# Optimization experiments

Hardware: AMD Instinct MI355X
Metric: run time of the kernel (lower is better)

## Reference

```python
import jax, jax.numpy as jnp
import numpy as np

N = 100000
E = 1600000
F_DIM = 128
H_DIM = 64
K_CLUSTERS = 16
NEG_SLOPE = 0.2


def setup_inputs() -> dict:
    key = jax.random.key(0)
    ks = jax.random.split(key, 10)
    X = jax.random.normal(ks[0], (N, F_DIM), dtype=jnp.float32)
    ei_feat = jax.random.randint(ks[1], (2, E), 0, N, dtype=jnp.int64)
    batch = jnp.zeros((N,), dtype=jnp.int64)
    # GATv2Conv layer 1 params (heads=1): lin_l, lin_r [F,H], att [H], bias [H]
    s1 = 1.0 / np.sqrt(F_DIM)
    W1l = jax.random.uniform(ks[2], (F_DIM, H_DIM), jnp.float32, -s1, s1)
    W1r = jax.random.uniform(ks[3], (F_DIM, H_DIM), jnp.float32, -s1, s1)
    a1 = jax.random.uniform(ks[4], (H_DIM,), jnp.float32, -1/np.sqrt(H_DIM), 1/np.sqrt(H_DIM))
    b1 = jnp.zeros((H_DIM,), jnp.float32)
    # layer 2: [H,K]
    s2 = 1.0 / np.sqrt(H_DIM)
    W2l = jax.random.uniform(ks[5], (H_DIM, K_CLUSTERS), jnp.float32, -s2, s2)
    W2r = jax.random.uniform(ks[6], (H_DIM, K_CLUSTERS), jnp.float32, -s2, s2)
    a2 = jax.random.uniform(ks[7], (K_CLUSTERS,), jnp.float32, -1/np.sqrt(K_CLUSTERS), 1/np.sqrt(K_CLUSTERS))
    b2 = jnp.zeros((K_CLUSTERS,), jnp.float32)
    return {"X": X, "ei_feat": ei_feat, "batch": batch,
            "W1l": W1l, "W1r": W1r, "a1": a1, "b1": b1,
            "W2l": W2l, "W2r": W2r, "a2": a2, "b2": b2}


def gatv2_conv(x, src, dst, Wl, Wr, a, b, n_nodes):
    # GATv2 (heads=1): e_ij = a^T LeakyReLU(Wl x_j + Wr x_i); softmax over j->i; out_i = sum alpha * Wl x_j
    xl = x @ Wl            # [N,H] source transform
    xr = x @ Wr            # [N,H] target transform
    e = jax.nn.leaky_relu(xl[src] + xr[dst], NEG_SLOPE) @ a   # [E']
    m = jax.ops.segment_max(e, dst, num_segments=n_nodes)      # stable softmax per target
    w = jnp.exp(e - m[dst])
    denom = jax.ops.segment_sum(w, dst, num_segments=n_nodes)
    alpha = w / denom[dst]  # every node has a self-loop, so denom > 0
    out = jax.ops.segment_sum(alpha[:, None] * xl[src], dst, num_segments=n_nodes)
    return out + b


def reference(X, ei_feat, batch, W1l, W1r, a1, b1, W2l, W2r, a2, b2):
    loop = jnp.arange(N, dtype=ei_feat.dtype)
    src = jnp.concatenate([ei_feat[0], loop])  # add_self_loops=True (PyG default)
    dst = jnp.concatenate([ei_feat[1], loop])
    h = jax.nn.elu(gatv2_conv(X, src, dst, W1l, W1r, a1, b1, N))
    z = gatv2_conv(h, src, dst, W2l, W2r, a2, b2, N)
    return jax.nn.softmax(z, axis=1)
```

## Files before the change

### kernel.cpp

```cpp
#include <hip/hip_runtime.h>
#include <stdint.h>

#define F_DIM 128
#define H_DIM 64
#define K_DIM 16
#define BUK_SH 8
#define NCH 256

typedef _Float16 half2v __attribute__((ext_vector_type(2)));
typedef _Float16 half4 __attribute__((ext_vector_type(4)));
typedef _Float16 f16x8 __attribute__((ext_vector_type(8)));
typedef float f32x4 __attribute__((ext_vector_type(4)));

__global__ __launch_bounds__(256) void k_hist(const int* __restrict__ dst,
                                              int* __restrict__ hist,
                                              int E, int CH, int NBUK) {
    __shared__ int h[512];
    int t = threadIdx.x, c = blockIdx.x;
    for (int i = t; i < NBUK; i += 256) h[i] = 0;
    __syncthreads();
    int s = c * CH, e = min(s + CH, E);
    for (int i = s + t; i < e; i += 256) atomicAdd(&h[dst[i] >> BUK_SH], 1);
    __syncthreads();
    for (int i = t; i < NBUK; i += 256) hist[i * NCH + c] = h[i];
}

__global__ __launch_bounds__(256) void k_scanBkt(int* __restrict__ hist,
                                                 int* __restrict__ bktTot) {
    __shared__ int sh[256];
    int b = blockIdx.x, t = threadIdx.x;
    int v = hist[b * NCH + t];
    sh[t] = v;
    __syncthreads();
    for (int off = 1; off < 256; off <<= 1) {
        int x = (t >= off) ? sh[t - off] : 0;
        __syncthreads();
        sh[t] += x;
        __syncthreads();
    }
    hist[b * NCH + t] = sh[t] - v;
    if (t == 255) bktTot[b] = sh[255];
}

__global__ __launch_bounds__(256) void k_scanTot(const int* __restrict__ bktTot,
                                                 int* __restrict__ bktBase, int NBUK) {
    __shared__ int sh[256];
    int t = threadIdx.x;
    int i0 = 2 * t, i1 = 2 * t + 1;
    int v0 = (i0 < NBUK) ? bktTot[i0] : 0;
    int v1 = (i1 < NBUK) ? bktTot[i1] : 0;
    int s = v0 + v1;
    sh[t] = s;
    __syncthreads();
    for (int off = 1; off < 256; off <<= 1) {
        int x = (t >= off) ? sh[t - off] : 0;
        __syncthreads();
        sh[t] += x;
        __syncthreads();
    }
    int excl = sh[t] - s;
    if (i0 < NBUK) bktBase[i0] = excl;
    if (i1 < NBUK) bktBase[i1] = excl + v0;
    if (t == 255) bktBase[NBUK] = sh[255];
}

__global__ __launch_bounds__(256) void k_scatter(const int* __restrict__ src,
                                                 const int* __restrict__ dst,
                                                 const int* __restrict__ hist,
                                                 const int* __restrict__ bktBase,
                                                 uint32_t* __restrict__ binned,
                                                 int E, int CH, int NBUK) {
    __shared__ int ctr[512];
    int t = threadIdx.x, c = blockIdx.x;
    for (int i = t; i < NBUK; i += 256) ctr[i] = bktBase[i] + hist[i * NCH + c];
    __syncthreads();
    int s = c * CH, e = min(s + CH, E);
    for (int i = s + t; i < e; i += 256) {
        int d = dst[i];
        int pos = atomicAdd(&ctr[d >> BUK_SH], 1);
        binned[pos] = (uint32_t)src[i] | ((uint32_t)(d & 255) << 20);
    }
}

__global__ __launch_bounds__(256) void k_fine2(const uint32_t* __restrict__ binned,
                                               const int* __restrict__ bktBase,
                                               int* __restrict__ rowptr,
                                               int* __restrict__ col, int N) {
    __shared__ int h[256], sc[256], slotL[256];
    int b = blockIdx.x, t = threadIdx.x;
    int n0 = b << BUK_SH;
    int s = bktBase[b], e = bktBase[b + 1];
    h[t] = 0;
    __syncthreads();
    for (int i = s + t; i < e; i += 256) atomicAdd(&h[binned[i] >> 20], 1);
    __syncthreads();
    int v = h[t];
    sc[t] = v;
    __syncthreads();
    for (int off = 1; off < 256; off <<= 1) {
        int x = (t >= off) ? sc[t - off] : 0;
        __syncthreads();
        sc[t] += x;
        __syncthreads();
    }
    int excl = sc[t] - v;
    int n = n0 + t;
    int rowbase = s + n0;
    if (n < N) {
        int rp = rowbase + excl + t;
        rowptr[n] = rp;
        col[rp] = n;
        slotL[t] = rp + 1;
        if (n == N - 1) rowptr[N] = rp + v + 1;
    }
    __syncthreads();
    for (int i = s + t; i < e; i += 256) {
        uint32_t p = binned[i];
        int pos = atomicAdd(&slotL[p >> 20], 1);
        col[pos] = (int)(p & 0xFFFFFu);
    }
}

__global__ __launch_bounds__(256) void k_gemm1m(
        const float* __restrict__ X,
        const float* __restrict__ W1l, const float* __restrict__ W1r,
        _Float16* __restrict__ xlh, _Float16* __restrict__ xrh, int N) {
    __shared__ _Float16 Ws[16384];
    __shared__ _Float16 Xs[128 * 136];
    int t = threadIdx.x;
    int n0 = blockIdx.x * 128;
    int validRows = N - n0; if (validRows > 128) validRows = 128;
    for (int i = t; i < 4096; i += 256) {
        int k = i >> 5, c4 = (i & 31) << 2;
        float4 v = (c4 < 64) ? *(const float4*)&W1l[k * 64 + c4]
                             : *(const float4*)&W1r[k * 64 + (c4 - 64)];
        int s = k >> 5, q = (k >> 3) & 3, j = k & 7;
        float vv[4] = {v.x, v.y, v.z, v.w};
#pragma unroll
        for (int u = 0; u < 4; ++u) {
            int C = c4 + u, c = C >> 4, n = C & 15;
            Ws[(((c * 4 + s) * 4 + q) * 16 + n) * 8 + j] = (_Float16)vv[u];
        }
    }
    for (int i = t; i < 4096; i += 256) {
        int r = i >> 5, c4 = (i & 31) << 2;
        float4 v = {0.f, 0.f, 0.f, 0.f};
        if (r < validRows) v = *(const float4*)&X[(long)(n0 + r) * 128 + c4];
        half4 hv;
        hv.x = (_Float16)v.x; hv.y = (_Float16)v.y;
        hv.z = (_Float16)v.z; hv.w = (_Float16)v.w;
        *(half4*)&Xs[r * 136 + c4] = hv;
    }
    __syncthreads();
    int w = t >> 6, lane = t & 63;
    int m = lane & 15, q = lane >> 4;
    f32x4 acc[2][8];
#pragma unroll
    for (int a = 0; a < 2; ++a)
#pragma unroll
        for (int c = 0; c < 8; ++c) acc[a][c] = (f32x4){0.f, 0.f, 0.f, 0.f};
#pragma unroll
    for (int s = 0; s < 4; ++s) {
        f16x8 a0 = *(const f16x8*)&Xs[(w * 32 + m) * 136 + s * 32 + q * 8];
        f16x8 a1 = *(const f16x8*)&Xs[(w * 32 + 16 + m) * 136 + s * 32 + q * 8];
#pragma unroll
        for (int c = 0; c < 8; ++c) {
            f16x8 b = *(const f16x8*)&Ws[(((c * 4 + s) * 4 + q) * 16 + m) * 8];
            acc[0][c] = __builtin_amdgcn_mfma_f32_16x16x32_f16(a0, b, acc[0][c], 0, 0, 0);
            acc[1][c] = __builtin_amdgcn_mfma_f32_16x16x32_f16(a1, b, acc[1][c], 0, 0, 0);
        }
    }
#pragma unroll
    for (int sub = 0; sub < 2; ++sub)
#pragma unroll
    for (int c = 0; c < 8; ++c)
#pragma unroll
    for (int r = 0; r < 4; ++r) {
        int gn = n0 + w * 32 + sub * 16 + q * 4 + r;
        if (gn < N) {
            int C = c * 16 + m;
            _Float16 v = (_Float16)acc[sub][c][r];
            if (C < 64) xlh[(long)gn * 64 + C] = v;
            else        xrh[(long)gn * 64 + (C - 64)] = v;
        }
    }
}

__global__ __launch_bounds__(256) void k_gemm2m(
        const _Float16* __restrict__ Hm,
        const float* __restrict__ W2l, const float* __restrict__ W2r,
        _Float16* __restrict__ xlh, _Float16* __restrict__ xrh, int N) {
    __shared__ _Float16 Ws2[2048];
    __shared__ _Float16 Hs[256 * 72];
    int t = threadIdx.x;
    int n0 = blockIdx.x * 256;
    int validRows = N - n0; if (validRows > 256) validRows = 256;
    for (int i = t; i < 512; i += 256) {
        int k = i >> 3, c4 = (i & 7) << 2;
        float4 v = (c4 < 16) ? *(const float4*)&W2l[k * 16 + c4]
                             : *(const float4*)&W2r[k * 16 + (c4 - 16)];
        int s = k >> 5, q = (k >> 3) & 3, j = k & 7;
        float vv[4] = {v.x, v.y, v.z, v.w};
#pragma unroll
        for (int u = 0; u < 4; ++u) {
            int C = c4 + u, c = C >> 4, n = C & 15;
            Ws2[(((c * 2 + s) * 4 + q) * 16 + n) * 8 + j] = (_Float16)vv[u];
        }
    }
    for (int i = t; i < 2048; i += 256) {
        int r = i >> 3, c8 = (i & 7) << 3;
        f16x8 v = {0, 0, 0, 0, 0, 0, 0, 0};
        if (r < validRows) v = *(const f16x8*)&Hm[(long)(n0 + r) * 64 + c8];
        *(f16x8*)&Hs[r * 72 + c8] = v;
    }
    __syncthreads();
    int w = t >> 6, lane = t & 63;
    int m = lane & 15, q = lane >> 4;
    f32x4 acc[4][2];
#pragma unroll
    for (int a = 0; a < 4; ++a)
#pragma unroll
        for (int c = 0; c < 2; ++c) acc[a][c] = (f32x4){0.f, 0.f, 0.f, 0.f};
#pragma unroll
    for (int s = 0; s < 2; ++s) {
        f16x8 a[4];
#pragma unroll
        for (int sub = 0; sub < 4; ++sub)
            a[sub] = *(const f16x8*)&Hs[(w * 64 + sub * 16 + m) * 72 + s * 32 + q * 8];
#pragma unroll
        for (int c = 0; c < 2; ++c) {
            f16x8 b = *(const f16x8*)&Ws2[(((c * 2 + s) * 4 + q) * 16 + m) * 8];
#pragma unroll
            for (int sub = 0; sub < 4; ++sub)
                acc[sub][c] = __builtin_amdgcn_mfma_f32_16x16x32_f16(a[sub], b, acc[sub][c], 0, 0, 0);
        }
    }
#pragma unroll
    for (int sub = 0; sub < 4; ++sub)
#pragma unroll
    for (int c = 0; c < 2; ++c)
#pragma unroll
    for (int r = 0; r < 4; ++r) {
        int gn = n0 + w * 64 + sub * 16 + q * 4 + r;
        if (gn < N) {
            int C = c * 16 + m;
            _Float16 v = (_Float16)acc[sub][c][r];
            if (C < 16) xlh[(long)gn * 16 + C] = v;
            else        xrh[(long)gn * 16 + (C - 16)] = v;
        }
    }
}

__global__ void k_att1(const f16x8* __restrict__ xlh, const f16x8* __restrict__ xrh,
                       const float* __restrict__ a1, const float* __restrict__ b1,
                       const int* __restrict__ rowptr, const int* __restrict__ col,
                       f16x8* __restrict__ hout, int N) {
    int n = (int)((blockIdx.x * (unsigned)blockDim.x + threadIdx.x) >> 4);
    int lane = threadIdx.x & 63;
    if (n >= N) return;
    int q = lane & 7;
    int g = (lane >> 3) & 1;
    float4 af0 = ((const float4*)a1)[q * 2 + 0];
    float4 af1 = ((const float4*)a1)[q * 2 + 1];
    half2v a01 = {(_Float16)af0.x, (_Float16)af0.y};
    half2v a23 = {(_Float16)af0.z, (_Float16)af0.w};
    half2v a45 = {(_Float16)af1.x, (_Float16)af1.y};
    half2v a67 = {(_Float16)af1.z, (_Float16)af1.w};
    f16x8 xrv = xrh[(long)n * 8 + q];
    int jb = rowptr[n], je = rowptr[n + 1];
    float l = 0.f;
    float o[8] = {0.f, 0.f, 0.f, 0.f, 0.f, 0.f, 0.f, 0.f};
    int j = jb + g;
    for (; j + 2 < je; j += 4) {
        int s0 = col[j], s1 = col[j + 2];
        f16x8 xh0 = xlh[(long)s0 * 8 + q];
        f16x8 xh1 = xlh[(long)s1 * 8 + q];
        f16x8 t0 = xh0 + xrv, t1 = xh1 + xrv;
        f16x8 u0 = __builtin_elementwise_max(t0, t0 * (_Float16)0.2f);
        f16x8 u1 = __builtin_elementwise_max(t1, t1 * (_Float16)0.2f);
        half2v u0a = {u0[0], u0[1]}, u0b = {u0[2], u0[3]}, u0c = {u0[4], u0[5]}, u0d = {u0[6], u0[7]};
        half2v u1a = {u1[0], u1[1]}, u1b = {u1[2], u1[3]}, u1c = {u1[4], u1[5]}, u1d = {u1[6], u1[7]};
        float e0 = __builtin_amdgcn_fdot2(u0a, a01,
                    __builtin_amdgcn_fdot2(u0b, a23,
                     __builtin_amdgcn_fdot2(u0c, a45,
                      __builtin_amdgcn_fdot2(u0d, a67, 0.f, false), false), false), false);
        float e1 = __builtin_amdgcn_fdot2(u1a, a01,
                    __builtin_amdgcn_fdot2(u1b, a23,
                     __builtin_amdgcn_fdot2(u1c, a45,
                      __builtin_amdgcn_fdot2(u1d, a67, 0.f, false), false), false), false);
#pragma unroll
        for (int off = 1; off < 8; off <<= 1) {
            e0 += __shfl_xor(e0, off, 8);
            e1 += __shfl_xor(e1, off, 8);
        }
        float c0 = __expf(e0), c1 = __expf(e1);
        l += c0 + c1;
#pragma unroll
        for (int i = 0; i < 8; ++i)
            o[i] = fmaf(c0, (float)xh0[i], fmaf(c1, (float)xh1[i], o[i]));
    }
    for (; j < je; j += 2) {
        int s = col[j];
        f16x8 xh = xlh[(long)s * 8 + q];
        f16x8 t = xh + xrv;
        f16x8 u = __builtin_elementwise_max(t, t * (_Float16)0.2f);
        half2v ua = {u[0], u[1]}, ub = {u[2], u[3]}, uc = {u[4], u[5]}, ud = {u[6], u[7]};
        float e = __builtin_amdgcn_fdot2(ua, a01,
                   __builtin_amdgcn_fdot2(ub, a23,
                    __builtin_amdgcn_fdot2(uc, a45,
                     __builtin_amdgcn_fdot2(ud, a67, 0.f, false), false), false), false);
#pragma unroll
        for (int off = 1; off < 8; off <<= 1) e += __shfl_xor(e, off, 8);
        float c = __expf(e);
        l += c;
#pragma unroll
        for (int i = 0; i < 8; ++i) o[i] = fmaf(c, (float)xh[i], o[i]);
    }
    l += __shfl_xor(l, 8);
#pragma unroll
    for (int i = 0; i < 8; ++i) o[i] += __shfl_xor(o[i], 8);
    if (g == 0) {
        float4 bv0 = ((const float4*)b1)[q * 2 + 0];
        float4 bv1 = ((const float4*)b1)[q * 2 + 1];
        float bb[8] = {bv0.x, bv0.y, bv0.z, bv0.w, bv1.x, bv1.y, bv1.z, bv1.w};
        float rl = 1.f / l;
        f16x8 hv;
#pragma unroll
        for (int i = 0; i < 8; ++i) {
            float h = o[i] * rl + bb[i];
            h = (h > 0.f) ? h : (__expf(h) - 1.f);
            hv[i] = (_Float16)h;
        }
        hout[(long)n * 8 + q] = hv;
    }
}

__global__ void k_att2(const half4* __restrict__ xlh, const half4* __restrict__ xrh,
                       const float* __restrict__ a2, const float* __restrict__ b2v,
                       const int* __restrict__ rowptr, const int* __restrict__ col,
                       float* __restrict__ out, int N) {
    int n = (int)((blockIdx.x * (unsigned)blockDim.x + threadIdx.x) >> 4);
    int lane = threadIdx.x & 63;
    if (n >= N) return;
    int q = lane & 3;
    int g = (lane >> 2) & 3;
    float4 af = ((const float4*)a2)[q];
    half2v alo = {(_Float16)af.x, (_Float16)af.y};
    half2v ahi = {(_Float16)af.z, (_Float16)af.w};
    half4 xrv = xrh[(long)n * 4 + q];
    int jb = rowptr[n], je = rowptr[n + 1];
    float l = 0.f;
    float4 o = {0.f, 0.f, 0.f, 0.f};
    int j = jb + g;
    for (; j + 4 < je; j += 8) {
        int s0 = col[j], s1 = col[j + 4];
        half4 xh0 = xlh[(long)s0 * 4 + q];
        half4 xh1 = xlh[(long)s1 * 4 + q];
        half4 t0 = xh0 + xrv, t1 = xh1 + xrv;
        half4 u0 = __builtin_elementwise_max(t0, t0 * (_Float16)0.2f);
        half4 u1 = __builtin_elementwise_max(t1, t1 * (_Float16)0.2f);
        half2v u0lo = {u0.x, u0.y}, u0hi = {u0.z, u0.w};
        half2v u1lo = {u1.x, u1.y}, u1hi = {u1.z, u1.w};
        float e0 = __builtin_amdgcn_fdot2(u0lo, alo,
                    __builtin_amdgcn_fdot2(u0hi, ahi, 0.f, false), false);
        float e1 = __builtin_amdgcn_fdot2(u1lo, alo,
                    __builtin_amdgcn_fdot2(u1hi, ahi, 0.f, false), false);
        e0 += __shfl_xor(e0, 1, 4); e0 += __shfl_xor(e0, 2, 4);
        e1 += __shfl_xor(e1, 1, 4); e1 += __shfl_xor(e1, 2, 4);
        float c0 = __expf(e0), c1 = __expf(e1);
        l += c0 + c1;
        o.x = fmaf(c0, (float)xh0.x, fmaf(c1, (float)xh1.x, o.x));
        o.y = fmaf(c0, (float)xh0.y, fmaf(c1, (float)xh1.y, o.y));
        o.z = fmaf(c0, (float)xh0.z, fmaf(c1, (float)xh1.z, o.z));
        o.w = fmaf(c0, (float)xh0.w, fmaf(c1, (float)xh1.w, o.w));
    }
    for (; j < je; j += 4) {
        int s = col[j];
        half4 xh = xlh[(long)s * 4 + q];
        half4 t = xh + xrv;
        half4 u = __builtin_elementwise_max(t, t * (_Float16)0.2f);
        half2v ulo = {u.x, u.y}, uhi = {u.z, u.w};
        float e = __builtin_amdgcn_fdot2(ulo, alo,
                   __builtin_amdgcn_fdot2(uhi, ahi, 0.f, false), false);
        e += __shfl_xor(e, 1, 4);
        e += __shfl_xor(e, 2, 4);
        float c = __expf(e);
        l += c;
        o.x = fmaf(c, (float)xh.x, o.x);
        o.y = fmaf(c, (float)xh.y, o.y);
        o.z = fmaf(c, (float)xh.z, o.z);
        o.w = fmaf(c, (float)xh.w, o.w);
    }
#pragma unroll
    for (int off = 4; off <= 8; off <<= 1) {
        l   += __shfl_xor(l, off);
        o.x += __shfl_xor(o.x, off);
        o.y += __shfl_xor(o.y, off);
        o.z += __shfl_xor(o.z, off);
        o.w += __shfl_xor(o.w, off);
    }
    if (g == 0) {
        float4 bv = ((const float4*)b2v)[q];
        float rl = 1.f / l;
        float4 z;
        z.x = o.x * rl + bv.x;
        z.y = o.y * rl + bv.y;
        z.z = o.z * rl + bv.z;
        z.w = o.w * rl + bv.w;
        float mx = fmaxf(fmaxf(z.x, z.y), fmaxf(z.z, z.w));
        mx = fmaxf(mx, __shfl_xor(mx, 1, 4));
        mx = fmaxf(mx, __shfl_xor(mx, 2, 4));
        float4 ez;
        ez.x = __expf(z.x - mx); ez.y = __expf(z.y - mx);
        ez.z = __expf(z.z - mx); ez.w = __expf(z.w - mx);
        float ss = ez.x + ez.y + ez.z + ez.w;
        ss += __shfl_xor(ss, 1, 4);
        ss += __shfl_xor(ss, 2, 4);
        float rs = 1.f / ss;
        ez.x *= rs; ez.y *= rs; ez.z *= rs; ez.w *= rs;
        ((float4*)out)[(long)n * 4 + q] = ez;
    }
}

extern "C" void kernel_launch(void* const* d_in, const int* in_sizes, int n_in,
                              void* d_out, int out_size, void* d_ws, size_t ws_size,
                              hipStream_t stream) {
    const float* X   = (const float*)d_in[0];
    const int*   ei  = (const int*)d_in[1];
    const float* W1l = (const float*)d_in[3];
    const float* W1r = (const float*)d_in[4];
    const float* a1  = (const float*)d_in[5];
    const float* b1  = (const float*)d_in[6];
    const float* W2l = (const float*)d_in[7];
    const float* W2r = (const float*)d_in[8];
    const float* a2  = (const float*)d_in[9];
    const float* b2  = (const float*)d_in[10];

    int N = in_sizes[0] / F_DIM;
    int E = in_sizes[1] / 2;
    int M = E + N;
    int NBUK = (N + 255) >> BUK_SH;
    int NH = NBUK * NCH;
    int CH = (E + NCH - 1) / NCH;
    const int* srcv = ei;
    const int* dstv = ei + E;

    char* w = (char*)d_ws;
    size_t off = 0;
    auto alloc = [&](size_t bytes) -> char* {
        char* p = w + off;
        off = (off + bytes + 255) & ~(size_t)255;
        return p;
    };
    int* rowptr  = (int*)alloc((size_t)(N + 1) * sizeof(int));
    int* hist    = (int*)alloc((size_t)NH * sizeof(int));
    int* bktTot  = (int*)alloc((size_t)NBUK * sizeof(int));
    int* bktBase = (int*)alloc((size_t)(NBUK + 1) * sizeof(int));
    int* col     = (int*)alloc((size_t)M * sizeof(int));
    uint32_t* binned = (uint32_t*)alloc((size_t)E * sizeof(uint32_t));
    _Float16* xl1h = (_Float16*)alloc((size_t)N * H_DIM * 2);
    _Float16* xr1h = (_Float16*)alloc((size_t)N * H_DIM * 2);
    _Float16* h1h  = (_Float16*)alloc((size_t)N * H_DIM * 2);
    _Float16* xl2h = (_Float16*)alloc((size_t)N * K_DIM * 2);
    _Float16* xr2h = (_Float16*)alloc((size_t)N * K_DIM * 2);

    k_hist<<<NCH, 256, 0, stream>>>(dstv, hist, E, CH, NBUK);
    k_scanBkt<<<NBUK, 256, 0, stream>>>(hist, bktTot);
    k_scanTot<<<1, 256, 0, stream>>>(bktTot, bktBase, NBUK);
    k_scatter<<<NCH, 256, 0, stream>>>(srcv, dstv, hist, bktBase, binned, E, CH, NBUK);
    k_fine2<<<NBUK, 256, 0, stream>>>(binned, bktBase, rowptr, col, N);

    int g1Blocks = (N + 127) / 128;
    k_gemm1m<<<g1Blocks, 256, 0, stream>>>(X, W1l, W1r, xl1h, xr1h, N);
    int nodeBlocks16 = (N + 15) / 16;
    k_att1<<<nodeBlocks16, 256, 0, stream>>>((const f16x8*)xl1h, (const f16x8*)xr1h,
                                             a1, b1, rowptr, col, (f16x8*)h1h, N);
    int g2Blocks = (N + 255) / 256;
    k_gemm2m<<<g2Blocks, 256, 0, stream>>>(h1h, W2l, W2r, xl2h, xr2h, N);
    k_att2<<<nodeBlocks16, 256, 0, stream>>>((const half4*)xl2h, (const half4*)xr2h,
                                             a2, b2, rowptr, col, (float*)d_out, N);
}
```

Baseline: 247.1 us.

## Pre-swizzle weights once, load GEMM operands directly, and vectorize output stores

A new small kernel converts and swizzles both layers' weights to fp16 once into global memory, so each GEMM block no longer rebuilds the weight tile in LDS. The GEMM kernels now load activation fragments straight from global memory into registers instead of staging them through shared memory. This also removes the __syncthreads barrier. Outputs go through a per-wave LDS transpose so rows are written with 16-byte vector stores instead of scattered 2-byte stores. The trade-offs are one extra launch, weight reads coming from global/L2 per wave, and less coalesced direct X loads.

```diff
diff --git a/kernel.cpp b/kernel.cpp
--- a/kernel.cpp
+++ b/kernel.cpp
@@ -121,132 +121,149 @@
     }
 }
 
+__global__ __launch_bounds__(256) void k_swzW(const float* __restrict__ W1l,
+                                              const float* __restrict__ W1r,
+                                              const float* __restrict__ W2l,
+                                              const float* __restrict__ W2r,
+                                              _Float16* __restrict__ Wg1,
+                                              _Float16* __restrict__ Wg2) {
+    int t = threadIdx.x;
+    if (blockIdx.x == 0) {
+        for (int i = t; i < 4096; i += 256) {
+            int k = i >> 5, c4 = (i & 31) << 2;
+            float4 v = (c4 < 64) ? *(const float4*)&W1l[k * 64 + c4]
+                                 : *(const float4*)&W1r[k * 64 + (c4 - 64)];
+            int s = k >> 5, q = (k >> 3) & 3, j = k & 7;
+            float vv[4] = {v.x, v.y, v.z, v.w};
+#pragma unroll
+            for (int u = 0; u < 4; ++u) {
+                int C = c4 + u, c = C >> 4, n = C & 15;
+                Wg1[(((c * 4 + s) * 4 + q) * 16 + n) * 8 + j] = (_Float16)vv[u];
+            }
+        }
+    } else {
+        for (int i = t; i < 512; i += 256) {
+            int k = i >> 3, c4 = (i & 7) << 2;
+            float4 v = (c4 < 16) ? *(const float4*)&W2l[k * 16 + c4]
+                                 : *(const float4*)&W2r[k * 16 + (c4 - 16)];
+            int s = k >> 5, q = (k >> 3) & 3, j = k & 7;
+            float vv[4] = {v.x, v.y, v.z, v.w};
+#pragma unroll
+            for (int u = 0; u < 4; ++u) {
+                int C = c4 + u, c = C >> 4, n = C & 15;
+                Wg2[(((c * 2 + s) * 4 + q) * 16 + n) * 8 + j] = (_Float16)vv[u];
+            }
+        }
+    }
+}
+
 __global__ __launch_bounds__(256) void k_gemm1m(
-        const float* __restrict__ X,
-        const float* __restrict__ W1l, const float* __restrict__ W1r,
+        const float* __restrict__ X, const _Float16* __restrict__ Wg,
         _Float16* __restrict__ xlh, _Float16* __restrict__ xrh, int N) {
-    __shared__ _Float16 Ws[16384];
-    __shared__ _Float16 Xs[128 * 136];
+    __shared__ _Float16 T[4][32 * 136];
     int t = threadIdx.x;
     int n0 = blockIdx.x * 128;
-    int validRows = N - n0; if (validRows > 128) validRows = 128;
-    for (int i = t; i < 4096; i += 256) {
-        int k = i >> 5, c4 = (i & 31) << 2;
-        float4 v = (c4 < 64) ? *(const float4*)&W1l[k * 64 + c4]
-                             : *(const float4*)&W1r[k * 64 + (c4 - 64)];
-        int s = k >> 5, q = (k >> 3) & 3, j = k & 7;
-        float vv[4] = {v.x, v.y, v.z, v.w};
-#pragma unroll
-        for (int u = 0; u < 4; ++u) {
-            int C = c4 + u, c = C >> 4, n = C & 15;
-            Ws[(((c * 4 + s) * 4 + q) * 16 + n) * 8 + j] = (_Float16)vv[u];
-        }
-    }
-    for (int i = t; i < 4096; i += 256) {
-        int r = i >> 5, c4 = (i & 31) << 2;
-        float4 v = {0.f, 0.f, 0.f, 0.f};
-        if (r < validRows) v = *(const float4*)&X[(long)(n0 + r) * 128 + c4];
-        half4 hv;
-        hv.x = (_Float16)v.x; hv.y = (_Float16)v.y;
-        hv.z = (_Float16)v.z; hv.w = (_Float16)v.w;
-        *(half4*)&Xs[r * 136 + c4] = hv;
-    }
-    __syncthreads();
-    int w = t >> 6, lane = t & 63;
-    int m = lane & 15, q = lane >> 4;
+    int w = t >> 6, lane = t & 63, m = lane & 15, q = lane >> 4;
+    int r0 = n0 + w * 32 + m;
+    int r1 = r0 + 16;
+    bool v0 = r0 < N, v1 = r1 < N;
+    const float* p0 = X + (long)r0 * 128 + q * 8;
+    const float* p1 = X + (long)r1 * 128 + q * 8;
     f32x4 acc[2][8];
 #pragma unroll
     for (int a = 0; a < 2; ++a)
 #pragma unroll
         for (int c = 0; c < 8; ++c) acc[a][c] = (f32x4){0.f, 0.f, 0.f, 0.f};
+    const float4 z4 = {0.f, 0.f, 0.f, 0.f};
 #pragma unroll
     for (int s = 0; s < 4; ++s) {
-        f16x8 a0 = *(const f16x8*)&Xs[(w * 32 + m) * 136 + s * 32 + q * 8];
-        f16x8 a1 = *(const f16x8*)&Xs[(w * 32 + 16 + m) * 136 + s * 32 + q * 8];
+        float4 xa = v0 ? *(const float4*)(p0 + s * 32)     : z4;
+        float4 xb = v0 ? *(const float4*)(p0 + s * 32 + 4) : z4;
+        float4 ya = v1 ? *(const float4*)(p1 + s * 32)     : z4;
+        float4 yb = v1 ? *(const float4*)(p1 + s * 32 + 4) : z4;
+        f16x8 a0, a1;
+        a0[0] = (_Float16)xa.x; a0[1] = (_Float16)xa.y;
+        a0[2] = (_Float16)xa.z; a0[3] = (_Float16)xa.w;
+        a0[4] = (_Float16)xb.x; a0[5] = (_Float16)xb.y;
+        a0[6] = (_Float16)xb.z; a0[7] = (_Float16)xb.w;
+        a1[0] = (_Float16)ya.x; a1[1] = (_Float16)ya.y;
+        a1[2] = (_Float16)ya.z; a1[3] = (_Float16)ya.w;
+        a1[4] = (_Float16)yb.x; a1[5] = (_Float16)yb.y;
+        a1[6] = (_Float16)yb.z; a1[7] = (_Float16)yb.w;
 #pragma unroll
         for (int c = 0; c < 8; ++c) {
-            f16x8 b = *(const f16x8*)&Ws[(((c * 4 + s) * 4 + q) * 16 + m) * 8];
+            f16x8 b = *(const f16x8*)&Wg[(((c * 4 + s) * 4 + q) * 16 + m) * 8];
             acc[0][c] = __builtin_amdgcn_mfma_f32_16x16x32_f16(a0, b, acc[0][c], 0, 0, 0);
             acc[1][c] = __builtin_amdgcn_mfma_f32_16x16x32_f16(a1, b, acc[1][c], 0, 0, 0);
         }
     }
+    _Float16* Tw = T[w];
 #pragma unroll
     for (int sub = 0; sub < 2; ++sub)
 #pragma unroll
     for (int c = 0; c < 8; ++c)
 #pragma unroll
-    for (int r = 0; r < 4; ++r) {
-        int gn = n0 + w * 32 + sub * 16 + q * 4 + r;
+    for (int r = 0; r < 4; ++r)
+        Tw[(sub * 16 + q * 4 + r) * 136 + c * 16 + m] = (_Float16)acc[sub][c][r];
+#pragma unroll
+    for (int p = 0; p < 4; ++p) {
+        int lr = p * 8 + (lane >> 3);
+        int cg = (lane & 7) * 8;
+        f16x8 v = *(const f16x8*)&Tw[lr * 136 + cg];
+        int gn = n0 + w * 32 + lr;
         if (gn < N) {
-            int C = c * 16 + m;
-            _Float16 v = (_Float16)acc[sub][c][r];
-            if (C < 64) xlh[(long)gn * 64 + C] = v;
-            else        xrh[(long)gn * 64 + (C - 64)] = v;
+            if (cg < 64) *(f16x8*)&xlh[(long)gn * 64 + cg] = v;
+            else         *(f16x8*)&xrh[(long)gn * 64 + (cg - 64)] = v;
         }
     }
 }
 
 __global__ __launch_bounds__(256) void k_gemm2m(
-        const _Float16* __restrict__ Hm,
-        const float* __restrict__ W2l, const float* __restrict__ W2r,
+        const _Float16* __restrict__ Hm, const _Float16* __restrict__ Wg2,
         _Float16* __restrict__ xlh, _Float16* __restrict__ xrh, int N) {
-    __shared__ _Float16 Ws2[2048];
-    __shared__ _Float16 Hs[256 * 72];
+    __shared__ _Float16 T[4][64 * 40];
     int t = threadIdx.x;
     int n0 = blockIdx.x * 256;
-    int validRows = N - n0; if (validRows > 256) validRows = 256;
-    for (int i = t; i < 512; i += 256) {
-        int k = i >> 3, c4 = (i & 7) << 2;
-        float4 v = (c4 < 16) ? *(const float4*)&W2l[k * 16 + c4]
-                             : *(const float4*)&W2r[k * 16 + (c4 - 16)];
-        int s = k >> 5, q = (k >> 3) & 3, j = k & 7;
-        float vv[4] = {v.x, v.y, v.z, v.w};
-#pragma unroll
-        for (int u = 0; u < 4; ++u) {
-            int C = c4 + u, c = C >> 4, n = C & 15;
-            Ws2[(((c * 2 + s) * 4 + q) * 16 + n) * 8 + j] = (_Float16)vv[u];
-        }
-    }
-    for (int i = t; i < 2048; i += 256) {
-        int r = i >> 3, c8 = (i & 7) << 3;
-        f16x8 v = {0, 0, 0, 0, 0, 0, 0, 0};
-        if (r < validRows) v = *(const f16x8*)&Hm[(long)(n0 + r) * 64 + c8];
-        *(f16x8*)&Hs[r * 72 + c8] = v;
-    }
-    __syncthreads();
-    int w = t >> 6, lane = t & 63;
-    int m = lane & 15, q = lane >> 4;
+    int w = t >> 6, lane = t & 63, m = lane & 15, q = lane >> 4;
     f32x4 acc[4][2];
 #pragma unroll
     for (int a = 0; a < 4; ++a)
 #pragma unroll
         for (int c = 0; c < 2; ++c) acc[a][c] = (f32x4){0.f, 0.f, 0.f, 0.f};
+    const f16x8 zh = {0, 0, 0, 0, 0, 0, 0, 0};
 #pragma unroll
     for (int s = 0; s < 2; ++s) {
         f16x8 a[4];
 #pragma unroll
-        for (int sub = 0; sub < 4; ++sub)
-            a[sub] = *(const f16x8*)&Hs[(w * 64 + sub * 16 + m) * 72 + s * 32 + q * 8];
+        for (int sub = 0; sub < 4; ++sub) {
+            int row = n0 + w * 64 + sub * 16 + m;
+            a[sub] = (row < N) ? *(const f16x8*)&Hm[(long)row * 64 + s * 32 + q * 8] : zh;
+        }
 #pragma unroll
         for (int c = 0; c < 2; ++c) {
-            f16x8 b = *(const f16x8*)&Ws2[(((c * 2 + s) * 4 + q) * 16 + m) * 8];
+            f16x8 b = *(const f16x8*)&Wg2[(((c * 2 + s) * 4 + q) * 16 + m) * 8];
 #pragma unroll
             for (int sub = 0; sub < 4; ++sub)
                 acc[sub][c] = __builtin_amdgcn_mfma_f32_16x16x32_f16(a[sub], b, acc[sub][c], 0, 0, 0);
         }
     }
+    _Float16* Tw = T[w];
 #pragma unroll
     for (int sub = 0; sub < 4; ++sub)
 #pragma unroll
     for (int c = 0; c < 2; ++c)
 #pragma unroll
-    for (int r = 0; r < 4; ++r) {
-        int gn = n0 + w * 64 + sub * 16 + q * 4 + r;
+    for (int r = 0; r < 4; ++r)
+        Tw[(sub * 16 + q * 4 + r) * 40 + c * 16 + m] = (_Float16)acc[sub][c][r];
+#pragma unroll
+    for (int p = 0; p < 4; ++p) {
+        int lr = p * 16 + (lane >> 2);
+        int cg = (lane & 3) * 8;
+        f16x8 v = *(const f16x8*)&Tw[lr * 40 + cg];
+        int gn = n0 + w * 64 + lr;
         if (gn < N) {
-            int C = c * 16 + m;
-            _Float16 v = (_Float16)acc[sub][c][r];
-            if (C < 16) xlh[(long)gn * 16 + C] = v;
-            else        xrh[(long)gn * 16 + (C - 16)] = v;
+            if (cg < 16) *(f16x8*)&xlh[(long)gn * 16 + cg] = v;
+            else         *(f16x8*)&xrh[(long)gn * 16 + (cg - 16)] = v;
         }
     }
 }
@@ -463,7 +480,10 @@
     _Float16* h1h  = (_Float16*)alloc((size_t)N * H_DIM * 2);
     _Float16* xl2h = (_Float16*)alloc((size_t)N * K_DIM * 2);
     _Float16* xr2h = (_Float16*)alloc((size_t)N * K_DIM * 2);
-
+    _Float16* Wg1  = (_Float16*)alloc((size_t)16384 * 2);
+    _Float16* Wg2  = (_Float16*)alloc((size_t)2048 * 2);
+
+    k_swzW<<<2, 256, 0, stream>>>(W1l, W1r, W2l, W2r, Wg1, Wg2);
     k_hist<<<NCH, 256, 0, stream>>>(dstv, hist, E, CH, NBUK);
     k_scanBkt<<<NBUK, 256, 0, stream>>>(hist, bktTot);
     k_scanTot<<<1, 256, 0, stream>>>(bktTot, bktBase, NBUK);
@@ -471,12 +491,12 @@
     k_fine2<<<NBUK, 256, 0, stream>>>(binned, bktBase, rowptr, col, N);
 
     int g1Blocks = (N + 127) / 128;
-    k_gemm1m<<<g1Blocks, 256, 0, stream>>>(X, W1l, W1r, xl1h, xr1h, N);
+    k_gemm1m<<<g1Blocks, 256, 0, stream>>>(X, Wg1, xl1h, xr1h, N);
     int nodeBlocks16 = (N + 15) / 16;
     k_att1<<<nodeBlocks16, 256, 0, stream>>>((const f16x8*)xl1h, (const f16x8*)xr1h,
                                              a1, b1, rowptr, col, (f16x8*)h1h, N);
     int g2Blocks = (N + 255) / 256;
-    k_gemm2m<<<g2Blocks, 256, 0, stream>>>(h1h, W2l, W2r, xl2h, xr2h, N);
+    k_gemm2m<<<g2Blocks, 256, 0, stream>>>(h1h, Wg2, xl2h, xr2h, N);
     k_att2<<<nodeBlocks16, 256, 0, stream>>>((const half4*)xl2h, (const half4*)xr2h,
                                              a2, b2, rowptr, col, (float*)d_out, N);
 }
```

Result: slower. 262.2 us (+6.1%).
